# Kernel optimization log

Measured on AMD Instinct MI355X. Metric: run time of the kernel, lower is better.

Reference implementation:

```python
import jax, jax.numpy as jnp
import numpy as np
from jax import lax

B, T_ENC, H, E, OUT, STEPS = 32, 128, 512, 512, 256, 16
SOS = 1.0


def _gru_layer(x, h0, Wi, Wh, bi, bh):
    # x: [T, B, in], h0: [B, H] -> (ys [T, B, H], hT [B, H])
    def step(h, xt):
        gi = xt @ Wi.T + bi
        gh = h @ Wh.T + bh
        ir, iz, inn = jnp.split(gi, 3, axis=-1)
        hr, hz, hn = jnp.split(gh, 3, axis=-1)
        r = jax.nn.sigmoid(ir + hr)
        z = jax.nn.sigmoid(iz + hz)
        n = jnp.tanh(inn + r * hn)
        hnew = (1.0 - z) * n + z * h
        return hnew, hnew
    hT, ys = lax.scan(step, h0, x)
    return ys, hT


def setup_inputs() -> dict:
    key = jax.random.key(0)
    ks = jax.random.split(key, 20)
    p = lambda k, s: jax.random.normal(k, s, jnp.float32) * 0.05
    return {
        "enc_outputs": jax.random.normal(ks[0], (B, T_ENC, H), jnp.float32),
        "hidden_state": jax.random.normal(ks[1], (2, B, H), jnp.float32),
        "target": jax.random.normal(ks[2], (STEPS, B, OUT), jnp.float32),
        "Wq": p(ks[3], (H, H)),
        "Wk": p(ks[4], (H, H)),
        "wv": p(ks[5], (H,)),
        "emb_W": p(ks[6], (E, OUT)),
        "emb_b": p(ks[7], (E,)),
        "gru_Wi0": p(ks[8], (3 * H, E + H)),
        "gru_Wh0": p(ks[9], (3 * H, H)),
        "gru_bi0": p(ks[10], (3 * H,)),
        "gru_bh0": p(ks[11], (3 * H,)),
        "gru_Wi1": p(ks[12], (3 * H, H)),
        "gru_Wh1": p(ks[13], (3 * H, H)),
        "gru_bi1": p(ks[14], (3 * H,)),
        "gru_bh1": p(ks[15], (3 * H,)),
        "last_W": p(ks[16], (OUT, E)),
        "last_b": p(ks[17], (OUT,)),
        "teacher_mask": jax.random.randint(ks[18], (STEPS, B), 0, 2).astype(jnp.int32),
        "num_steps": STEPS,
    }


def reference(enc_outputs, hidden_state, target, Wq, Wk, wv, emb_W, emb_b,
              gru_Wi0, gru_Wh0, gru_bi0, gru_bh0,
              gru_Wi1, gru_Wh1, gru_bi1, gru_bh1,
              last_W, last_b, teacher_mask, num_steps):
    emb = lambda x: x @ emb_W.T + emb_b
    kproj = enc_outputs @ Wk.T  # [B, T, H], key projection (constant across steps)
    b = enc_outputs.shape[0]
    out_dim = last_b.shape[0]
    inp = emb(jnp.ones((1, b, out_dim), enc_outputs.dtype)) * SOS  # [1, B, E]
    pre = [inp]
    hidden = hidden_state
    outs, attns = [], []
    for i in range(num_steps):
        q = hidden[-1][:, None, :] @ Wq.T                       # [B, 1, H]
        feat = jnp.tanh(q[:, :, None, :] + kproj[:, None, :, :])  # [B, 1, T, H]
        scores = feat @ wv                                      # [B, 1, T]
        w = jax.nn.softmax(scores, axis=-1)
        context = w @ enc_outputs                               # [B, 1, H]
        emb_pre = jnp.concatenate(pre, axis=0).transpose(1, 0, 2)  # [B, i+1, E]
        ctx = jnp.broadcast_to(context, (b, emb_pre.shape[1], context.shape[2]))
        x = jnp.concatenate([ctx, emb_pre], axis=-1).transpose(1, 0, 2)  # [i+1, B, H+E]
        y0, h0 = _gru_layer(x, hidden[0], gru_Wi0, gru_Wh0, gru_bi0, gru_bh0)
        y1, h1 = _gru_layer(y0, hidden[1], gru_Wi1, gru_Wh1, gru_bi1, gru_bh1)
        hidden = jnp.stack([h0, h1])
        lin = y1[-1] @ last_W.T + last_b                        # [B, OUT]
        forced = jnp.where(teacher_mask[i][:, None] != 0, target[i], lin)
        inp = emb(forced)[None]                                 # [1, B, E]
        pre.append(inp)
        outs.append(forced[None])
        attns.append(w)
    outputs = jnp.concatenate(outs, axis=0)   # [num_steps, B, OUT]
    attn_w = jnp.stack(attns)                 # [num_steps, B, 1, T]
    return outputs, hidden, attn_w
```

## Files before the change

kernel.cpp:

```cpp
#include <hip/hip_runtime.h>
#include <math.h>

#define B 32
#define T 128
#define H 512
#define E 512
#define ODIM 256
#define STEPS 16
#define G3 1536
#define BH (B * H)

typedef float4 f4;
typedef unsigned int uint32;
typedef unsigned short ushort;

__device__ __forceinline__ float sigmoidf_(float x) { return 1.0f / (1.0f + __expf(-x)); }
__device__ __forceinline__ float tanh_fast(float x) {
    float t = __expf(-2.0f * fabsf(x));
    float r = (1.0f - t) / (1.0f + t);
    return __builtin_copysignf(r, x);
}
__device__ __forceinline__ float dot4(const f4 a, const f4 b) {
    return fmaf(a.x, b.x, fmaf(a.y, b.y, fmaf(a.z, b.z, a.w * b.w)));
}
__device__ __forceinline__ void bf2x(uint32 v, float& lo, float& hi) {
    union { uint32 u; float f; } a, b;
    a.u = v << 16; b.u = v & 0xffff0000u;
    lo = a.f; hi = b.f;
}
__device__ __forceinline__ float dot8bf(uint4 wv, const f4 hA, const f4 hB) {
    float w0, w1, w2, w3, w4, w5, w6, w7;
    bf2x(wv.x, w0, w1); bf2x(wv.y, w2, w3); bf2x(wv.z, w4, w5); bf2x(wv.w, w6, w7);
    float s = fmaf(w0, hA.x, w1 * hA.y);
    s = fmaf(w2, hA.z, s); s = fmaf(w3, hA.w, s);
    s = fmaf(w4, hB.x, s); s = fmaf(w5, hB.y, s);
    s = fmaf(w6, hB.z, s); s = fmaf(w7, hB.w, s);
    return s;
}
__device__ __forceinline__ ushort f2bf(float f) {
    union { float f; uint32 u; } a; a.f = f;
    uint32 r = a.u + 0x7fffu + ((a.u >> 16) & 1u);
    return (ushort)(r >> 16);
}

#define A0(kq, b) ((kq) * 4 + ((kq) >> 3) + (b))
#define ST4_SZ 544
__device__ __forceinline__ void stage4(const float* __restrict__ src, float* __restrict__ st,
                                       int tid) {
    f4* d = (f4*)st;
    const f4* s = (const f4*)src;
    for (int idx = tid; idx < 512; idx += 256) {
        int b = idx >> 7, kq = idx & 127;
        d[A0(kq, b)] = s[idx];
    }
}

__device__ __forceinline__ void stage_b32(const float* __restrict__ src, float* __restrict__ st,
                                          int tid, int nthr) {
    f4* d = (f4*)st;
    const f4* s = (const f4*)src;
    for (int idx = tid; idx < 4096; idx += nthr) {
        int b = idx >> 7, kq = idx & 127;
        d[kq * 32 + (b ^ (kq & 31))] = s[idx];
    }
}
__device__ __forceinline__ f4 ldb32(const float* __restrict__ st, int kq, int b) {
    return ((const f4*)st)[kq * 32 + (b ^ (kq & 31))];
}

__global__ void cvt_bf16_kernel(const float* __restrict__ src, ushort* __restrict__ dst, int n4) {
    int i = blockIdx.x * 256 + threadIdx.x;
    if (i < n4) {
        f4 v = ((const f4*)src)[i];
        ushort4 o;
        o.x = f2bf(v.x); o.y = f2bf(v.y); o.z = f2bf(v.z); o.w = f2bf(v.w);
        ((ushort4*)dst)[i] = o;
    }
}

__global__ void transpose_kernel(const float* __restrict__ in, float* __restrict__ out,
                                 int R, int C, int ldin) {
    __shared__ float tile[32][33];
    int r0 = blockIdx.x * 32, c0 = blockIdx.y * 32;
    int tx = threadIdx.x & 31, ty = threadIdx.x >> 5;
#pragma unroll
    for (int k = 0; k < 4; ++k) {
        int r = r0 + ty + k * 8;
        tile[ty + k * 8][tx] = in[(size_t)r * ldin + c0 + tx];
    }
    __syncthreads();
#pragma unroll
    for (int k = 0; k < 4; ++k) {
        int c = c0 + ty + k * 8;
        out[(size_t)c * R + r0 + tx] = tile[tx][ty + k * 8];
    }
}

__global__ void __launch_bounds__(256) kproj_gemm_kernel(const float* __restrict__ A,
                                                         const float* __restrict__ Bt,
                                                         float* __restrict__ kpT) {
    __shared__ float As[64][68];
    __shared__ float Bs[64][64];
    int r0 = blockIdx.x * 64, c0 = blockIdx.y * 64;
    int tid = threadIdx.x;
    int tx = tid & 15, ty = tid >> 4;
    float acc[4][4] = {};
    for (int k0 = 0; k0 < 512; k0 += 64) {
#pragma unroll
        for (int i = 0; i < 4; ++i) {
            int row = i * 16 + ty, col = tx * 4;
            f4 av = *(const f4*)(A + (size_t)(r0 + row) * 512 + k0 + col);
            As[row][col] = av.x; As[row][col + 1] = av.y; As[row][col + 2] = av.z; As[row][col + 3] = av.w;
            f4 bv = *(const f4*)(Bt + (size_t)(k0 + row) * 512 + c0 + col);
            *(f4*)&Bs[row][col] = bv;
        }
        __syncthreads();
#pragma unroll 8
        for (int kk = 0; kk < 64; ++kk) {
            float a[4];
#pragma unroll
            for (int i = 0; i < 4; ++i) a[i] = As[ty * 4 + i][kk];
            f4 bv = *(const f4*)&Bs[kk][tx * 4];
#pragma unroll
            for (int i = 0; i < 4; ++i) {
                acc[i][0] += a[i] * bv.x; acc[i][1] += a[i] * bv.y;
                acc[i][2] += a[i] * bv.z; acc[i][3] += a[i] * bv.w;
            }
        }
        __syncthreads();
    }
#pragma unroll
    for (int i = 0; i < 4; ++i) {
        int r = r0 + ty * 4 + i;
        int b = r >> 7, t = r & 127;
#pragma unroll
        for (int j = 0; j < 4; ++j) {
            int c = c0 + tx * 4 + j;
            kpT[((size_t)b * H + c) * T + t] = acc[i][j];
        }
    }
}

__global__ void __launch_bounds__(512) init_kernel(const float* __restrict__ hidden,
                                                   const float* __restrict__ emb_W,
                                                   const float* __restrict__ emb_b,
                                                   float* __restrict__ h0, float* __restrict__ h1,
                                                   float* __restrict__ inp) {
    int b = blockIdx.x, tid = threadIdx.x;
    h0[b * H + tid] = hidden[b * H + tid];
    h1[b * H + tid] = hidden[BH + b * H + tid];
    if (b == 0) {
        const f4* row = (const f4*)(emb_W + (size_t)tid * ODIM);
        float acc = emb_b[tid];
#pragma unroll 8
        for (int o = 0; o < 64; ++o) { f4 v = row[o]; acc += v.x + v.y + v.z + v.w; }
        for (int bb = 0; bb < B; ++bb) inp[bb * E + tid] = acc;
    }
}

__global__ void __launch_bounds__(256) attn1_kernel(
    int nb_q, const float* __restrict__ h1cur, const float* __restrict__ Wq,
    float* __restrict__ q, const float* __restrict__ last_W, const float* __restrict__ last_b,
    const float* __restrict__ target_step, const int* __restrict__ mask_step,
    float* __restrict__ f, float* __restrict__ out_step) {
    __shared__ float sh[16384];
    int tid = threadIdx.x;
    stage_b32(h1cur, sh, tid, 256);
    __syncthreads();
    if ((int)blockIdx.x < nb_q) {
        int jg = blockIdx.x * 8 + (tid & 7), b = tid >> 3;
        const f4* w = (const f4*)(Wq + (size_t)jg * H);
        float acc = 0.f;
#pragma unroll 8
        for (int kq = 0; kq < 128; ++kq) acc += dot4(w[kq], ldb32(sh, kq, b));
        q[b * H + jg] = acc;
    } else {
        int og = (blockIdx.x - nb_q) * 8 + (tid & 7), b = tid >> 3;
        const f4* w = (const f4*)(last_W + (size_t)og * H);
        float acc = 0.f;
#pragma unroll 8
        for (int kq = 0; kq < 128; ++kq) acc += dot4(w[kq], ldb32(sh, kq, b));
        float lin = acc + last_b[og];
        float ff = mask_step[b] ? target_step[b * ODIM + og] : lin;
        f[b * ODIM + og] = ff;
        out_step[b * ODIM + og] = ff;
    }
}

__global__ void __launch_bounds__(256) attn2_kernel(
    const float* __restrict__ q, const float* __restrict__ kpT, const float* __restrict__ wv,
    float* __restrict__ spart, const float* __restrict__ f, const float* __restrict__ emb_W,
    const float* __restrict__ emb_b, float* __restrict__ inp) {
    __shared__ float sm[8704];
    int tid = threadIdx.x;
    if ((int)blockIdx.x < 256) {
        int b = blockIdx.x >> 3, js = blockIdx.x & 7;
        float* qs = sm;
        float* ws_ = sm + 64;
        float* part = sm + 128;
        if (tid < 64) {
            qs[tid] = q[b * H + js * 64 + tid];
            ws_[tid] = wv[js * 64 + tid];
        }
        __syncthreads();
        int t = tid & 127, jh = tid >> 7;
        const float* kp = kpT + ((size_t)b * H + js * 64 + jh * 32) * T + t;
        float sa = 0.f;
#pragma unroll 8
        for (int jj = 0; jj < 32; ++jj) {
            int j = jh * 32 + jj;
            sa += tanh_fast(qs[j] + kp[(size_t)jj * T]) * ws_[j];
        }
        part[tid] = sa;
        __syncthreads();
        if (tid < 128) spart[((size_t)b * 8 + js) * T + tid] = part[tid] + part[128 + tid];
    } else {
        float* st = sm;
        {
            f4* d = (f4*)st;
            const f4* s = (const f4*)f;
            for (int idx = tid; idx < 2048; idx += 256) {
                int b = idx >> 6, oq = idx & 63;
                d[oq * 32 + (b ^ (oq & 31))] = s[idx];
            }
        }
        __syncthreads();
        int eg = (blockIdx.x - 256) * 16 + (tid & 15), bq = tid >> 4;
        const f4* w = (const f4*)(emb_W + (size_t)eg * ODIM);
        float a0 = 0.f, a1 = 0.f;
#pragma unroll 4
        for (int oq = 0; oq < 64; ++oq) {
            f4 wv_ = w[oq];
            a0 += dot4(wv_, ((const f4*)st)[oq * 32 + (bq ^ (oq & 31))]);
            a1 += dot4(wv_, ((const f4*)st)[oq * 32 + ((bq + 16) ^ (oq & 31))]);
        }
        float eb = emb_b[eg];
        inp[bq * E + eg] = a0 + eb;
        inp[(bq + 16) * E + eg] = a1 + eb;
    }
}

__global__ void __launch_bounds__(256) attn3_kernel(
    const float* __restrict__ spart, const float* __restrict__ enc,
    float* __restrict__ ctx, float* __restrict__ attn_out) {
    __shared__ float sw[T];
    __shared__ float red[4];
    __shared__ float part[256];
    int tid = threadIdx.x;
    int b = blockIdx.x >> 3, cs = blockIdx.x & 7;
    float sv = 0.f;
    if (tid < 128) {
        const float* sp = spart + (size_t)b * 8 * T + tid;
#pragma unroll
        for (int js = 0; js < 8; ++js) sv += sp[js * T];
        float m = sv;
        for (int off = 32; off; off >>= 1) m = fmaxf(m, __shfl_xor(m, off));
        if ((tid & 63) == 0) red[tid >> 6] = m;
    }
    __syncthreads();
    if (tid < 128) {
        float M = fmaxf(red[0], red[1]);
        float e = __expf(sv - M);
        sw[tid] = e;
        float s = e;
        for (int off = 32; off; off >>= 1) s += __shfl_xor(s, off);
        if ((tid & 63) == 0) red[2 + (tid >> 6)] = s;
    }
    __syncthreads();
    if (tid < 128) {
        float w = sw[tid] / (red[2] + red[3]);
        sw[tid] = w;
        if (cs == 0) attn_out[(size_t)b * T + tid] = w;
    }
    __syncthreads();
    int c = tid & 63, tq = tid >> 6;
    int cg = cs * 64 + c;
    const float* ep = enc + ((size_t)b * T + tq * 32) * H + cg;
    float acc = 0.f;
#pragma unroll 8
    for (int t2 = 0; t2 < 32; ++t2) acc += sw[tq * 32 + t2] * ep[(size_t)t2 * H];
    part[tid] = acc;
    __syncthreads();
    if (tid < 64) ctx[(size_t)b * H + cg] = part[tid] + part[64 + tid] + part[128 + tid] + part[192 + tid];
}

__global__ void __launch_bounds__(256) gi_kernel(
    const float* __restrict__ ctx, const float* __restrict__ inp,
    const ushort* __restrict__ Wi0bf, const float* __restrict__ bi0,
    float* __restrict__ gi_ctx, float* __restrict__ gi_emb_i) {
    __shared__ float sh[16384];
    int tid = threadIdx.x;
    bool isC = (int)blockIdx.x < 96;
    int lb = isC ? blockIdx.x : blockIdx.x - 96;
    stage_b32(isC ? ctx : inp, sh, tid, 256);
    __syncthreads();
    int cg = lb * 16 + (tid & 15), bq = tid >> 4;
    const uint4* w = (const uint4*)(Wi0bf + (size_t)cg * 1024 + (isC ? 0 : 512));
    float a0 = 0.f, a1 = 0.f;
#pragma unroll 4
    for (int it = 0; it < 64; ++it) {
        uint4 wv = w[it];
        f4 hA0 = ldb32(sh, it * 2, bq), hB0 = ldb32(sh, it * 2 + 1, bq);
        f4 hA1 = ldb32(sh, it * 2, bq + 16), hB1 = ldb32(sh, it * 2 + 1, bq + 16);
        a0 += dot8bf(wv, hA0, hB0);
        a1 += dot8bf(wv, hA1, hB1);
    }
    float bias = isC ? bi0[cg] : 0.f;
    float* dst = isC ? gi_ctx : gi_emb_i;
    dst[(size_t)bq * G3 + cg] = a0 + bias;
    dst[(size_t)(bq + 16) * G3 + cg] = a1 + bias;
}

__global__ void __launch_bounds__(256) cell_kernel(
    int nb0, const float* __restrict__ h0_src, float* __restrict__ h0_dst,
    const float* __restrict__ h1_src, float* __restrict__ h1_dst,
    const float* __restrict__ gi_emb_t, const float* __restrict__ gi_ctx,
    const ushort* __restrict__ Wh0bf, const float* __restrict__ bh0,
    const ushort* __restrict__ Wi1bf, const float* __restrict__ bi1,
    const ushort* __restrict__ Wh1bf, const float* __restrict__ bh1) {
    __shared__ __align__(16) float sh[7936];
    int tid = threadIdx.x;
    if ((int)blockIdx.x < nb0) {
        int jc = blockIdx.x & 31, bg = blockIdx.x >> 5;
        int j0 = jc * 16, b0 = bg * 4;
        stage4(h0_src + (size_t)b0 * H, sh, tid);
        __syncthreads();
        int j = tid & 15, ks = tid >> 4, jg = j0 + j;
        const uint4* w0 = (const uint4*)(Wh0bf + (size_t)jg * 512) + ks * 4;
        const uint4* w1 = (const uint4*)(Wh0bf + (size_t)(512 + jg) * 512) + ks * 4;
        const uint4* w2 = (const uint4*)(Wh0bf + (size_t)(1024 + jg) * 512) + ks * 4;
        float a0[4] = {}, a1[4] = {}, a2[4] = {};
#pragma unroll
        for (int c = 0; c < 4; ++c) {
            uint4 u0 = w0[c], u1 = w1[c], u2 = w2[c];
            int kq = ks * 8 + c * 2;
#pragma unroll
            for (int b = 0; b < 4; ++b) {
                f4 hA = ((const f4*)sh)[A0(kq, b)];
                f4 hB = ((const f4*)sh)[A0(kq + 1, b)];
                a0[b] += dot8bf(u0, hA, hB);
                a1[b] += dot8bf(u1, hA, hB);
                a2[b] += dot8bf(u2, hA, hB);
            }
        }
        float* part = sh + ST4_SZ * 4;
        {
            float* p = part + (size_t)tid * 13;
#pragma unroll
            for (int b = 0; b < 4; ++b) { p[b] = a0[b]; p[4 + b] = a1[b]; p[8 + b] = a2[b]; }
        }
        __syncthreads();
        if (tid < 64) {
            int fj = tid & 15, fb = tid >> 4;
            int jg2 = j0 + fj, bg2 = b0 + fb;
            float s0 = 0.f, s1 = 0.f, s2 = 0.f;
#pragma unroll
            for (int k2 = 0; k2 < 16; ++k2) {
                const float* p = part + (size_t)(k2 * 16 + fj) * 13;
                s0 += p[fb]; s1 += p[4 + fb]; s2 += p[8 + fb];
            }
            const float* gc = gi_ctx + (size_t)bg2 * G3;
            const float* ge = gi_emb_t + (size_t)bg2 * G3;
            float r_ = sigmoidf_(gc[jg2] + ge[jg2] + s0 + bh0[jg2]);
            float z_ = sigmoidf_(gc[H + jg2] + ge[H + jg2] + s1 + bh0[H + jg2]);
            float n_ = tanh_fast(gc[2 * H + jg2] + ge[2 * H + jg2] + r_ * (s2 + bh0[2 * H + jg2]));
            f4 hp = ((const f4*)sh)[A0(jg2 >> 2, fb)];
            float hprev = ((const float*)&hp)[jg2 & 3];
            h0_dst[(size_t)bg2 * H + jg2] = (1.f - z_) * n_ + z_ * hprev;
        }
    } else {
        int lb = blockIdx.x - nb0;
        int jc = lb & 31, bg = lb >> 5;
        int j0 = jc * 16, b0 = bg * 4;
        float* stX = sh;
        float* stH = sh + ST4_SZ * 4;
        stage4(h0_src + (size_t)b0 * H, stX, tid);
        stage4(h1_src + (size_t)b0 * H, stH, tid);
        __syncthreads();
        int j = tid & 15, ks = (tid >> 4) & 7, m = tid >> 7, jg = j0 + j;
        const ushort* Wm = m ? Wh1bf : Wi1bf;
        const float* stm = m ? stH : stX;
        const uint4* w0 = (const uint4*)(Wm + (size_t)jg * 512) + ks * 8;
        const uint4* w1 = (const uint4*)(Wm + (size_t)(512 + jg) * 512) + ks * 8;
        const uint4* w2 = (const uint4*)(Wm + (size_t)(1024 + jg) * 512) + ks * 8;
        float a0[4] = {}, a1[4] = {}, a2[4] = {};
#pragma unroll
        for (int c = 0; c < 8; ++c) {
            uint4 u0 = w0[c], u1 = w1[c], u2 = w2[c];
            int kq = ks * 16 + c * 2;
#pragma unroll
            for (int b = 0; b < 4; ++b) {
                f4 hA = ((const f4*)stm)[A0(kq, b)];
                f4 hB = ((const f4*)stm)[A0(kq + 1, b)];
                a0[b] += dot8bf(u0, hA, hB);
                a1[b] += dot8bf(u1, hA, hB);
                a2[b] += dot8bf(u2, hA, hB);
            }
        }
        float* part = sh + ST4_SZ * 8;
        {
            float* p = part + (size_t)tid * 13;
#pragma unroll
            for (int b = 0; b < 4; ++b) { p[b] = a0[b]; p[4 + b] = a1[b]; p[8 + b] = a2[b]; }
        }
        __syncthreads();
        if (tid < 64) {
            int fj = tid & 15, fb = tid >> 4;
            int jg2 = j0 + fj, bg2 = b0 + fb;
            float i0 = 0.f, i1 = 0.f, i2 = 0.f, g0 = 0.f, g1 = 0.f, g2 = 0.f;
#pragma unroll
            for (int k2 = 0; k2 < 8; ++k2) {
                const float* pi = part + (size_t)(k2 * 16 + fj) * 13;
                const float* ph = part + (size_t)((128 + k2 * 16 + fj)) * 13;
                i0 += pi[fb]; i1 += pi[4 + fb]; i2 += pi[8 + fb];
                g0 += ph[fb]; g1 += ph[4 + fb]; g2 += ph[8 + fb];
            }
            float r_ = sigmoidf_(i0 + bi1[jg2] + g0 + bh1[jg2]);
            float z_ = sigmoidf_(i1 + bi1[H + jg2] + g1 + bh1[H + jg2]);
            float n_ = tanh_fast(i2 + bi1[2 * H + jg2] + r_ * (g2 + bh1[2 * H + jg2]));
            f4 hp = ((const f4*)stH)[A0(jg2 >> 2, fb)];
            float hprev = ((const float*)&hp)[jg2 & 3];
            h1_dst[(size_t)bg2 * H + jg2] = (1.f - z_) * n_ + z_ * hprev;
        }
    }
}

__global__ void copy_hidden_kernel(const float* __restrict__ h0, const float* __restrict__ h1,
                                   float* __restrict__ dst) {
    int i = blockIdx.x * 256 + threadIdx.x;
    dst[i] = h0[i];
    dst[BH + i] = h1[i];
}

extern "C" void kernel_launch(void* const* d_in, const int* in_sizes, int n_in,
                              void* d_out_v, int out_size, void* d_ws, size_t ws_size,
                              hipStream_t stream) {
    const float* enc = (const float*)d_in[0];
    const float* hidden = (const float*)d_in[1];
    const float* target = (const float*)d_in[2];
    const float* Wq = (const float*)d_in[3];
    const float* Wk = (const float*)d_in[4];
    const float* wv = (const float*)d_in[5];
    const float* emb_W = (const float*)d_in[6];
    const float* emb_b = (const float*)d_in[7];
    const float* Wi0 = (const float*)d_in[8];
    const float* Wh0 = (const float*)d_in[9];
    const float* bi0 = (const float*)d_in[10];
    const float* bh0 = (const float*)d_in[11];
    const float* Wi1 = (const float*)d_in[12];
    const float* Wh1 = (const float*)d_in[13];
    const float* bi1 = (const float*)d_in[14];
    const float* bh1 = (const float*)d_in[15];
    const float* last_W = (const float*)d_in[16];
    const float* last_b = (const float*)d_in[17];
    const int* tmask = (const int*)d_in[18];

    float* out = (float*)d_out_v;
    float* out_hidden = out + (size_t)STEPS * B * ODIM;
    float* out_attn = out_hidden + (size_t)2 * BH;

    float* ws = (float*)d_ws;
    float* kpT = ws;
    float* WkT = kpT + 2097152;
    float* gi_emb = WkT + 262144;
    float* gi_ctx = gi_emb + 786432;
    float* h0buf = gi_ctx + 49152;
    float* h1buf = h0buf + 32768;
    float* qbuf = h1buf + 32768;
    float* ctxbuf = qbuf + 16384;
    float* fbuf = ctxbuf + 16384;
    float* inpbuf = fbuf + 8192;
    float* spart = inpbuf + 16384;
    ushort* Wi0bf = (ushort*)(spart + 32768);
    ushort* Wh0bf = Wi0bf + 1572864;
    ushort* Wi1bf = Wh0bf + 786432;
    ushort* Wh1bf = Wi1bf + 786432;

    cvt_bf16_kernel<<<1536, 256, 0, stream>>>(Wi0, Wi0bf, 393216);
    cvt_bf16_kernel<<<768, 256, 0, stream>>>(Wh0, Wh0bf, 196608);
    cvt_bf16_kernel<<<768, 256, 0, stream>>>(Wi1, Wi1bf, 196608);
    cvt_bf16_kernel<<<768, 256, 0, stream>>>(Wh1, Wh1bf, 196608);

    transpose_kernel<<<dim3(16, 16), 256, 0, stream>>>(Wk, WkT, 512, 512, 512);
    kproj_gemm_kernel<<<dim3(64, 8), 256, 0, stream>>>(enc, WkT, kpT);
    init_kernel<<<B, 512, 0, stream>>>(hidden, emb_W, emb_b, h0buf, h1buf, inpbuf);

    int p0 = 0, p1 = 0;
    for (int i = 0; i < STEPS; ++i) {
        int im1 = (i > 0) ? i - 1 : 0;
        const float* h1cur = h1buf + (size_t)p1 * BH;
        attn1_kernel<<<(i > 0) ? 96 : 64, 256, 0, stream>>>(
            64, h1cur, Wq, qbuf, last_W, last_b, target + (size_t)im1 * B * ODIM,
            tmask + im1 * B, fbuf, out + (size_t)im1 * B * ODIM);
        attn2_kernel<<<(i > 0) ? 288 : 256, 256, 0, stream>>>(qbuf, kpT, wv, spart, fbuf,
                                                              emb_W, emb_b, inpbuf);
        attn3_kernel<<<256, 256, 0, stream>>>(spart, enc, ctxbuf, out_attn + (size_t)i * B * T);
        gi_kernel<<<192, 256, 0, stream>>>(ctxbuf, inpbuf, Wi0bf, bi0, gi_ctx,
                                           gi_emb + (size_t)i * B * G3);
        for (int t = 0; t <= i + 1; ++t) {
            int nb0 = (t <= i) ? 256 : 0;
            int nb1 = (t >= 1) ? 256 : 0;
            int tge = (t <= i) ? t : 0;
            cell_kernel<<<nb0 + nb1, 256, 0, stream>>>(
                nb0, h0buf + (size_t)p0 * BH, h0buf + (size_t)(p0 ^ 1) * BH,
                h1buf + (size_t)p1 * BH, h1buf + (size_t)(p1 ^ 1) * BH,
                gi_emb + (size_t)tge * B * G3, gi_ctx, Wh0bf, bh0, Wi1bf, bi1, Wh1bf, bh1);
            if (nb0) p0 ^= 1;
            if (nb1) p1 ^= 1;
        }
    }
    attn1_kernel<<<32, 256, 0, stream>>>(0, h1buf + (size_t)p1 * BH, Wq, qbuf, last_W, last_b,
                                         target + (size_t)15 * B * ODIM, tmask + 15 * B, fbuf,
                                         out + (size_t)15 * B * ODIM);
    copy_hidden_kernel<<<64, 256, 0, stream>>>(h0buf + (size_t)p0 * BH, h1buf + (size_t)p1 * BH,
                                               out_hidden);
}
```

Measured before the change: 2.508 ms.

## Retile GRU cell blocks to 8 columns by 8 batches and fuse bf16 conversions

The cell kernel now gives each block 8 hidden columns across 8 batch rows instead of 16 columns across 4 rows, so the grid still has 256 blocks per layer. Staged hidden state is duplicated into two halves. Each weight row is now loaded by half as many blocks, which is meant to cut global and L2 weight traffic in the per-timestep recurrent GEMV. The price is more shared memory per block and an extra barrier in the layer-1 path. Separately, the four weight-conversion launches are merged into one kernel to save launch overhead.

```diff
diff --git a/kernel.cpp b/kernel.cpp
--- a/kernel.cpp
+++ b/kernel.cpp
@@ -68,14 +68,22 @@
     return ((const f4*)st)[kq * 32 + (b ^ (kq & 31))];
 }
 
-__global__ void cvt_bf16_kernel(const float* __restrict__ src, ushort* __restrict__ dst, int n4) {
+__global__ void cvt4_bf16_kernel(const float* __restrict__ s0, ushort* __restrict__ d0,
+                                 const float* __restrict__ s1, ushort* __restrict__ d1,
+                                 const float* __restrict__ s2, ushort* __restrict__ d2,
+                                 const float* __restrict__ s3, ushort* __restrict__ d3) {
     int i = blockIdx.x * 256 + threadIdx.x;
-    if (i < n4) {
-        f4 v = ((const f4*)src)[i];
-        ushort4 o;
-        o.x = f2bf(v.x); o.y = f2bf(v.y); o.z = f2bf(v.z); o.w = f2bf(v.w);
-        ((ushort4*)dst)[i] = o;
-    }
+    const float* s;
+    ushort* d;
+    int off;
+    if (i < 393216) { s = s0; d = d0; off = i; }
+    else if (i < 589824) { s = s1; d = d1; off = i - 393216; }
+    else if (i < 786432) { s = s2; d = d2; off = i - 589824; }
+    else { s = s3; d = d3; off = i - 786432; }
+    f4 v = ((const f4*)s)[off];
+    ushort4 o;
+    o.x = f2bf(v.x); o.y = f2bf(v.y); o.z = f2bf(v.z); o.w = f2bf(v.w);
+    ((ushort4*)d)[off] = o;
 }
 
 __global__ void transpose_kernel(const float* __restrict__ in, float* __restrict__ out,
@@ -299,11 +307,11 @@
     float a0 = 0.f, a1 = 0.f;
 #pragma unroll 4
     for (int it = 0; it < 64; ++it) {
-        uint4 wv = w[it];
+        uint4 wv_ = w[it];
         f4 hA0 = ldb32(sh, it * 2, bq), hB0 = ldb32(sh, it * 2 + 1, bq);
         f4 hA1 = ldb32(sh, it * 2, bq + 16), hB1 = ldb32(sh, it * 2 + 1, bq + 16);
-        a0 += dot8bf(wv, hA0, hB0);
-        a1 += dot8bf(wv, hA1, hB1);
+        a0 += dot8bf(wv_, hA0, hB0);
+        a1 += dot8bf(wv_, hA1, hB1);
     }
     float bias = isC ? bi0[cg] : 0.f;
     float* dst = isC ? gi_ctx : gi_emb_i;
@@ -318,14 +326,18 @@
     const ushort* __restrict__ Wh0bf, const float* __restrict__ bh0,
     const ushort* __restrict__ Wi1bf, const float* __restrict__ bi1,
     const ushort* __restrict__ Wh1bf, const float* __restrict__ bh1) {
-    __shared__ __align__(16) float sh[7936];
+    __shared__ __align__(16) float sh[8704];
     int tid = threadIdx.x;
     if ((int)blockIdx.x < nb0) {
-        int jc = blockIdx.x & 31, bg = blockIdx.x >> 5;
-        int j0 = jc * 16, b0 = bg * 4;
-        stage4(h0_src + (size_t)b0 * H, sh, tid);
-        __syncthreads();
-        int j = tid & 15, ks = tid >> 4, jg = j0 + j;
+        int jc = blockIdx.x & 63, bg = blockIdx.x >> 6;
+        int j0 = jc * 8, b0 = bg * 8;
+        float* stA = sh;
+        float* stB = sh + 2176;
+        stage4(h0_src + (size_t)b0 * H, stA, tid);
+        stage4(h0_src + (size_t)(b0 + 4) * H, stB, tid);
+        __syncthreads();
+        int j = tid & 7, ks = (tid >> 3) & 15, bh = tid >> 7, jg = j0 + j;
+        const float* stm = bh ? stB : stA;
         const uint4* w0 = (const uint4*)(Wh0bf + (size_t)jg * 512) + ks * 4;
         const uint4* w1 = (const uint4*)(Wh0bf + (size_t)(512 + jg) * 512) + ks * 4;
         const uint4* w2 = (const uint4*)(Wh0bf + (size_t)(1024 + jg) * 512) + ks * 4;
@@ -334,60 +346,6 @@
         for (int c = 0; c < 4; ++c) {
             uint4 u0 = w0[c], u1 = w1[c], u2 = w2[c];
             int kq = ks * 8 + c * 2;
-#pragma unroll
-            for (int b = 0; b < 4; ++b) {
-                f4 hA = ((const f4*)sh)[A0(kq, b)];
-                f4 hB = ((const f4*)sh)[A0(kq + 1, b)];
-                a0[b] += dot8bf(u0, hA, hB);
-                a1[b] += dot8bf(u1, hA, hB);
-                a2[b] += dot8bf(u2, hA, hB);
-            }
-        }
-        float* part = sh + ST4_SZ * 4;
-        {
-            float* p = part + (size_t)tid * 13;
-#pragma unroll
-            for (int b = 0; b < 4; ++b) { p[b] = a0[b]; p[4 + b] = a1[b]; p[8 + b] = a2[b]; }
-        }
-        __syncthreads();
-        if (tid < 64) {
-            int fj = tid & 15, fb = tid >> 4;
-            int jg2 = j0 + fj, bg2 = b0 + fb;
-            float s0 = 0.f, s1 = 0.f, s2 = 0.f;
-#pragma unroll
-            for (int k2 = 0; k2 < 16; ++k2) {
-                const float* p = part + (size_t)(k2 * 16 + fj) * 13;
-                s0 += p[fb]; s1 += p[4 + fb]; s2 += p[8 + fb];
-            }
-            const float* gc = gi_ctx + (size_t)bg2 * G3;
-            const float* ge = gi_emb_t + (size_t)bg2 * G3;
-            float r_ = sigmoidf_(gc[jg2] + ge[jg2] + s0 + bh0[jg2]);
-            float z_ = sigmoidf_(gc[H + jg2] + ge[H + jg2] + s1 + bh0[H + jg2]);
-            float n_ = tanh_fast(gc[2 * H + jg2] + ge[2 * H + jg2] + r_ * (s2 + bh0[2 * H + jg2]));
-            f4 hp = ((const f4*)sh)[A0(jg2 >> 2, fb)];
-            float hprev = ((const float*)&hp)[jg2 & 3];
-            h0_dst[(size_t)bg2 * H + jg2] = (1.f - z_) * n_ + z_ * hprev;
-        }
-    } else {
-        int lb = blockIdx.x - nb0;
-        int jc = lb & 31, bg = lb >> 5;
-        int j0 = jc * 16, b0 = bg * 4;
-        float* stX = sh;
-        float* stH = sh + ST4_SZ * 4;
-        stage4(h0_src + (size_t)b0 * H, stX, tid);
-        stage4(h1_src + (size_t)b0 * H, stH, tid);
-        __syncthreads();
-        int j = tid & 15, ks = (tid >> 4) & 7, m = tid >> 7, jg = j0 + j;
-        const ushort* Wm = m ? Wh1bf : Wi1bf;
-        const float* stm = m ? stH : stX;
-        const uint4* w0 = (const uint4*)(Wm + (size_t)jg * 512) + ks * 8;
-        const uint4* w1 = (const uint4*)(Wm + (size_t)(512 + jg) * 512) + ks * 8;
-        const uint4* w2 = (const uint4*)(Wm + (size_t)(1024 + jg) * 512) + ks * 8;
-        float a0[4] = {}, a1[4] = {}, a2[4] = {};
-#pragma unroll
-        for (int c = 0; c < 8; ++c) {
-            uint4 u0 = w0[c], u1 = w1[c], u2 = w2[c];
-            int kq = ks * 16 + c * 2;
 #pragma unroll
             for (int b = 0; b < 4; ++b) {
                 f4 hA = ((const f4*)stm)[A0(kq, b)];
@@ -397,28 +355,91 @@
                 a2[b] += dot8bf(u2, hA, hB);
             }
         }
-        float* part = sh + ST4_SZ * 8;
+        float* part = sh + 4352;
         {
-            float* p = part + (size_t)tid * 13;
-#pragma unroll
-            for (int b = 0; b < 4; ++b) { p[b] = a0[b]; p[4 + b] = a1[b]; p[8 + b] = a2[b]; }
+            float* pr = part + (size_t)tid * 13;
+#pragma unroll
+            for (int b = 0; b < 4; ++b) { pr[b] = a0[b]; pr[4 + b] = a1[b]; pr[8 + b] = a2[b]; }
         }
         __syncthreads();
         if (tid < 64) {
-            int fj = tid & 15, fb = tid >> 4;
+            int fj = tid & 7, fb = tid >> 3;
+            int bh2 = fb >> 2, fbi = fb & 3;
+            int jg2 = j0 + fj, bg2 = b0 + fb;
+            float s0 = 0.f, s1 = 0.f, s2 = 0.f;
+#pragma unroll
+            for (int k2 = 0; k2 < 16; ++k2) {
+                const float* p = part + (size_t)(bh2 * 128 + k2 * 8 + fj) * 13;
+                s0 += p[fbi]; s1 += p[4 + fbi]; s2 += p[8 + fbi];
+            }
+            const float* gc = gi_ctx + (size_t)bg2 * G3;
+            const float* ge = gi_emb_t + (size_t)bg2 * G3;
+            float r_ = sigmoidf_(gc[jg2] + ge[jg2] + s0 + bh0[jg2]);
+            float z_ = sigmoidf_(gc[H + jg2] + ge[H + jg2] + s1 + bh0[H + jg2]);
+            float n_ = tanh_fast(gc[2 * H + jg2] + ge[2 * H + jg2] + r_ * (s2 + bh0[2 * H + jg2]));
+            const float* stm2 = (fb >= 4) ? stB : stA;
+            f4 hp = ((const f4*)stm2)[A0(jg2 >> 2, fb & 3)];
+            float hprev = ((const float*)&hp)[jg2 & 3];
+            h0_dst[(size_t)bg2 * H + jg2] = (1.f - z_) * n_ + z_ * hprev;
+        }
+    } else {
+        int lb = blockIdx.x - nb0;
+        int jc = lb & 63, bg = lb >> 6;
+        int j0 = jc * 8, b0 = bg * 8;
+        float* stX0 = sh;
+        float* stX1 = sh + 2176;
+        float* stH0 = sh + 4352;
+        float* stH1 = sh + 6528;
+        stage4(h0_src + (size_t)b0 * H, stX0, tid);
+        stage4(h0_src + (size_t)(b0 + 4) * H, stX1, tid);
+        stage4(h1_src + (size_t)b0 * H, stH0, tid);
+        stage4(h1_src + (size_t)(b0 + 4) * H, stH1, tid);
+        __syncthreads();
+        int j = tid & 7, ks = (tid >> 3) & 7, bh = (tid >> 6) & 1, m = tid >> 7, jg = j0 + j;
+        const float* stm = m ? (bh ? stH1 : stH0) : (bh ? stX1 : stX0);
+        const ushort* Wm = m ? Wh1bf : Wi1bf;
+        const uint4* w0 = (const uint4*)(Wm + (size_t)jg * 512) + ks * 8;
+        const uint4* w1 = (const uint4*)(Wm + (size_t)(512 + jg) * 512) + ks * 8;
+        const uint4* w2 = (const uint4*)(Wm + (size_t)(1024 + jg) * 512) + ks * 8;
+        float a0[4] = {}, a1[4] = {}, a2[4] = {};
+#pragma unroll
+        for (int c = 0; c < 8; ++c) {
+            uint4 u0 = w0[c], u1 = w1[c], u2 = w2[c];
+            int kq = ks * 16 + c * 2;
+#pragma unroll
+            for (int b = 0; b < 4; ++b) {
+                f4 hA = ((const f4*)stm)[A0(kq, b)];
+                f4 hB = ((const f4*)stm)[A0(kq + 1, b)];
+                a0[b] += dot8bf(u0, hA, hB);
+                a1[b] += dot8bf(u1, hA, hB);
+                a2[b] += dot8bf(u2, hA, hB);
+            }
+        }
+        __syncthreads();
+        float* part = sh;
+        {
+            float* pr = part + (size_t)tid * 13;
+#pragma unroll
+            for (int b = 0; b < 4; ++b) { pr[b] = a0[b]; pr[4 + b] = a1[b]; pr[8 + b] = a2[b]; }
+        }
+        __syncthreads();
+        if (tid < 64) {
+            int fj = tid & 7, fb = tid >> 3;
+            int bh2 = fb >> 2, fbi = fb & 3;
             int jg2 = j0 + fj, bg2 = b0 + fb;
             float i0 = 0.f, i1 = 0.f, i2 = 0.f, g0 = 0.f, g1 = 0.f, g2 = 0.f;
 #pragma unroll
             for (int k2 = 0; k2 < 8; ++k2) {
-                const float* pi = part + (size_t)(k2 * 16 + fj) * 13;
-                const float* ph = part + (size_t)((128 + k2 * 16 + fj)) * 13;
-                i0 += pi[fb]; i1 += pi[4 + fb]; i2 += pi[8 + fb];
-                g0 += ph[fb]; g1 += ph[4 + fb]; g2 += ph[8 + fb];
+                const float* pi = part + (size_t)(bh2 * 64 + k2 * 8 + fj) * 13;
+                const float* ph = part + (size_t)(128 + bh2 * 64 + k2 * 8 + fj) * 13;
+                i0 += pi[fbi]; i1 += pi[4 + fbi]; i2 += pi[8 + fbi];
+                g0 += ph[fbi]; g1 += ph[4 + fbi]; g2 += ph[8 + fbi];
             }
             float r_ = sigmoidf_(i0 + bi1[jg2] + g0 + bh1[jg2]);
             float z_ = sigmoidf_(i1 + bi1[H + jg2] + g1 + bh1[H + jg2]);
             float n_ = tanh_fast(i2 + bi1[2 * H + jg2] + r_ * (g2 + bh1[2 * H + jg2]));
-            f4 hp = ((const f4*)stH)[A0(jg2 >> 2, fb)];
+            const float* stm2 = (fb >= 4) ? stH1 : stH0;
+            f4 hp = ((const f4*)stm2)[A0(jg2 >> 2, fb & 3)];
             float hprev = ((const float*)&hp)[jg2 & 3];
             h1_dst[(size_t)bg2 * H + jg2] = (1.f - z_) * n_ + z_ * hprev;
         }
@@ -476,11 +497,7 @@
     ushort* Wi1bf = Wh0bf + 786432;
     ushort* Wh1bf = Wi1bf + 786432;
 
-    cvt_bf16_kernel<<<1536, 256, 0, stream>>>(Wi0, Wi0bf, 393216);
-    cvt_bf16_kernel<<<768, 256, 0, stream>>>(Wh0, Wh0bf, 196608);
-    cvt_bf16_kernel<<<768, 256, 0, stream>>>(Wi1, Wi1bf, 196608);
-    cvt_bf16_kernel<<<768, 256, 0, stream>>>(Wh1, Wh1bf, 196608);
-
+    cvt4_bf16_kernel<<<3840, 256, 0, stream>>>(Wi0, Wi0bf, Wh0, Wh0bf, Wi1, Wi1bf, Wh1, Wh1bf);
     transpose_kernel<<<dim3(16, 16), 256, 0, stream>>>(Wk, WkT, 512, 512, 512);
     kproj_gemm_kernel<<<dim3(64, 8), 256, 0, stream>>>(enc, WkT, kpT);
     init_kernel<<<B, 512, 0, stream>>>(hidden, emb_W, emb_b, h0buf, h1buf, inpbuf);
```

Result: slower. 5.980 ms (+138.4%).
